# Kernel tuning notes

Hardware: AMD Instinct MI355X
Metric: run time of the kernel (lower is better)

Reference implementation:

```python
import jax, jax.numpy as jnp
import numpy as np

B, C, RXD, E, P, OSIZE = 64, 4, 64, 512, 4, 256


def setup_inputs() -> dict:
    key = jax.random.key(0)
    ks = jax.random.split(key, 6)
    x = jax.random.normal(ks[0], (B, C, RXD, E), dtype=jnp.float32)
    # rxd permutation (gather form of the one-hot permuteRxdMatrix matmul)
    rxd_perm = jax.random.permutation(ks[1], RXD)
    # E permutation and its compositions: permuter = permuter @ permuteEMatrix
    # in column-index form: idx_{p+1}[j] = idx_p[e_perm[j]]
    e_perm = np.array(jax.random.permutation(ks[2], E))
    idx = e_perm.copy()
    cols = []
    for _ in range(P):
        cols.append(idx.copy())
        idx = idx[e_perm]
    e_idx = jnp.asarray(np.stack(cols, axis=1))  # (E, P) int
    # sign selected at the single nonzero entry of each permutation column
    signs = (jax.random.uniform(ks[3], (E, P)) > 0.5).astype(jnp.float32) * 2.0 - 1.0
    fan_in = RXD * E * P
    W = jax.random.normal(ks[4], (OSIZE, fan_in), dtype=jnp.float32) / np.float32(np.sqrt(fan_in))
    b = jax.random.normal(ks[5], (OSIZE,), dtype=jnp.float32) * 0.01
    return {"x": x, "rxd_perm": rxd_perm, "e_idx": e_idx, "signs": signs, "W": W, "b": b}


def reference(x, rxd_perm, e_idx, signs, W, b):
    Bb, Cc, R, Ee = x.shape
    Pp = e_idx.shape[1]
    # permute rxd axis (exact equivalent of x.transpose @ one-hot matrix)
    out = x[:, :, rxd_perm, :]                      # (B,C,R,E)
    # signed E-permutations for all P powers (exact equiv of dense matmul
    # with permuteETensor * signTensor, which has one signed nonzero per column)
    out = out[..., e_idx] * signs                   # (B,C,R,E,P)
    L = R * Ee
    pieces = []
    for p in range(Pp):
        k = 2 ** p
        v = out[..., p].reshape(Bb, Cc, L)
        if k == 1:
            pieces.append(v)                        # pool+unpool with k=1 is identity
        else:
            Lp = ((L + k - 1) // k) * k             # ceil_mode padding
            vp = jnp.pad(v, ((0, 0), (0, 0), (0, Lp - L)), constant_values=-jnp.inf)
            w = vp.reshape(Bb, Cc, Lp // k, k)
            am = jnp.argmax(w, axis=-1)             # first max, matching torch MaxPool1d
            mx = jnp.max(w, axis=-1)
            onehot = jnp.arange(k) == am[..., None]
            # MaxUnpool: max value at argmax position, zeros elsewhere
            pieces.append(jnp.where(onehot, mx[..., None], 0.0).reshape(Bb, Cc, Lp))
    pieces[-1] = pieces[-1][:, :, :L]               # truncate last piece to L
    cat = jnp.concatenate(pieces, axis=2)           # (B,C,L*P) since L % k == 0
    return cat @ W.T + b                            # (B,C,OSIZE)
```

## Files before the change

kernel.cpp:

```cpp
#include <hip/hip_runtime.h>
#include <stdint.h>

#define B_ 64
#define C_ 4
#define R_ 64
#define E_ 512
#define P_ 4
#define OS_ 256
#define L_ (R_*E_)
#define K_ (L_*E8_DUMMY)
#undef K_
#define K_ 131072
#define M_ 256

#define BM 256
#define BN 128
#define BK 32
#define Z_ 256
#define KCH (K_/Z_)
#define ITERS (KCH/BK)

typedef float  floatx4 __attribute__((ext_vector_type(4)));
typedef short  shortx8 __attribute__((ext_vector_type(8)));

#define GLDS16(g, l) __builtin_amdgcn_global_load_lds(                      \
    (const __attribute__((address_space(1))) void*)(g),                     \
    (__attribute__((address_space(3))) void*)(l), 16, 0, 0)

static __device__ __forceinline__ unsigned short f2bf(float f) {
  union { float f; unsigned int u; } v; v.f = f;
  unsigned int u = v.u;
  u += 0x7fffu + ((u >> 16) & 1u);
  return (unsigned short)(u >> 16);
}

__global__ __launch_bounds__(512) void prep(
    const float* __restrict__ x, const int* __restrict__ rxd_perm,
    const int* __restrict__ e_idx, const float* __restrict__ signs,
    const float* __restrict__ W,
    unsigned short* __restrict__ A2, unsigned short* __restrict__ W2) {
  __shared__ __align__(16) unsigned char smem[64 * 33 * 16];
  const int t = threadIdx.x;

  if (blockIdx.x < 2048) {
    const int blk = blockIdx.x;
    const int bcg = blk >> 6;
    const int r   = blk & 63;
    float (*xr)[E_] = (float(*)[E_])smem;
    const int pr = rxd_perm[r];

    #pragma unroll
    for (int i = 0; i < 2; ++i) {
      const int q   = i * 512 + t;
      const int row = q >> 7;
      const int c4  = q & 127;
      const int bc  = bcg * 8 + row;
      *(float4*)(&xr[row][c4 * 4]) =
          *(const float4*)(x + ((size_t)bc * R_ + pr) * E_ + c4 * 4);
    }
    __syncthreads();

    const int bcLoc = t >> 6;
    const int lane  = t & 63;
    const int e0    = lane * 8;
    const int bc    = bcg * 8 + bcLoc;
    const float* xp = xr[bcLoc];

    float v[4][8];
    #pragma unroll
    for (int i = 0; i < 8; ++i) {
      const uint4  ei = *(const uint4*)(e_idx + (size_t)(e0 + i) * 4);
      const float4 sg = *(const float4*)(signs + (size_t)(e0 + i) * 4);
      v[0][i] = xp[ei.x] * sg.x;
      v[1][i] = xp[ei.y] * sg.y;
      v[2][i] = xp[ei.z] * sg.z;
      v[3][i] = xp[ei.w] * sg.w;
    }

    const size_t gbase = (size_t)(r * 64 + lane) * 256 + bc;
    shortx8 o;

    #pragma unroll
    for (int i = 0; i < 8; ++i) o[i] = (short)f2bf(v[0][i]);
    *(shortx8*)(A2 + gbase * 8) = o;

    #pragma unroll
    for (int j = 0; j < 4; ++j) {
      const float a = v[1][2 * j], b = v[1][2 * j + 1];
      const bool first = (a >= b);
      o[2 * j]     = (short)f2bf(first ? a : 0.0f);
      o[2 * j + 1] = (short)f2bf(first ? 0.0f : b);
    }
    *(shortx8*)(A2 + (gbase + (size_t)4096 * 256) * 8) = o;

    #pragma unroll
    for (int j = 0; j < 2; ++j) {
      int am = 0; float m = v[2][4 * j];
      #pragma unroll
      for (int i = 1; i < 4; ++i)
        if (v[2][4 * j + i] > m) { m = v[2][4 * j + i]; am = i; }
      #pragma unroll
      for (int i = 0; i < 4; ++i) o[4 * j + i] = (short)f2bf(i == am ? m : 0.0f);
    }
    *(shortx8*)(A2 + (gbase + (size_t)2 * 4096 * 256) * 8) = o;

    {
      int am = 0; float m = v[3][0];
      #pragma unroll
      for (int i = 1; i < 8; ++i)
        if (v[3][i] > m) { m = v[3][i]; am = i; }
      #pragma unroll
      for (int i = 0; i < 8; ++i) o[i] = (short)f2bf(i == am ? m : 0.0f);
    }
    *(shortx8*)(A2 + (gbase + (size_t)3 * 4096 * 256) * 8) = o;

  } else {
    const int cb = blockIdx.x - 2048;
    const int nb = cb & 7;
    const int kb = cb >> 3;
    const int nbase  = nb * 32;
    const int k8base = kb * 64;
    unsigned short* T = (unsigned short*)smem;

    const int nloc = t >> 4, seg = t & 15;
    const float* wp = W + (size_t)(nbase + nloc) * K_ + (size_t)kb * 512 + seg * 32;
    #pragma unroll
    for (int j = 0; j < 4; ++j) {
      const float4 a0 = *(const float4*)(wp + j * 8);
      const float4 a1 = *(const float4*)(wp + j * 8 + 4);
      shortx8 g;
      g[0] = (short)f2bf(a0.x); g[1] = (short)f2bf(a0.y);
      g[2] = (short)f2bf(a0.z); g[3] = (short)f2bf(a0.w);
      g[4] = (short)f2bf(a1.x); g[5] = (short)f2bf(a1.y);
      g[6] = (short)f2bf(a1.z); g[7] = (short)f2bf(a1.w);
      const int k8loc = seg * 4 + j;
      *(shortx8*)(&T[(k8loc * 33 + nloc) * 8]) = g;
    }
    __syncthreads();

    const int k8loc = t >> 3, part = t & 7;
    unsigned short* wdst = W2 + ((size_t)(k8base + k8loc) * 256 + nbase) * 8;
    #pragma unroll
    for (int j = 0; j < 4; ++j) {
      const int g = j * 8 + part;
      *(shortx8*)(wdst + (size_t)g * 8) = *(const shortx8*)(&T[(k8loc * 33 + g) * 8]);
    }
  }
}

__global__ __launch_bounds__(512, 4) void gemm_splitk(
    const unsigned short* __restrict__ A2, const unsigned short* __restrict__ W2,
    float* __restrict__ Pp) {
  __shared__ unsigned short As[2][4 * 256 * 8];
  __shared__ unsigned short Ws[2][4 * 128 * 8];
  const int t    = threadIdx.x;
  const int lane = t & 63;
  const int wv   = t >> 6;

  const int id = blockIdx.x;
  const int ny = (id >> 3) & 1;
  const int z  = (id & 7) | ((id >> 4) << 3);
  const int nBase = ny * BN;

  const int wm   = (wv >> 1) * 64;
  const int wn   = (wv & 1) * 64;
  const int lrow = lane & 15;
  const int quad = lane >> 4;

  floatx4 acc[4][4];
  #pragma unroll
  for (int i = 0; i < 4; ++i)
    #pragma unroll
    for (int j = 0; j < 4; ++j) acc[i][j] = {0.f, 0.f, 0.f, 0.f};

  auto stage = [&](int buf, int it) {
    const size_t g0 = (size_t)(z * 64 + it * 4) * 256;
    #pragma unroll
    for (int c = 0; c < 2; ++c) {
      const int slot = (wv * 2 + c) * 64 + lane;
      GLDS16(A2 + (g0 + slot) * 8, &As[buf][slot * 8]);
    }
    const int wslot = wv * 64 + lane;
    const int slab  = wslot >> 7;
    const int nloc  = wslot & 127;
    GLDS16(W2 + (g0 + (size_t)slab * 256 + nBase + nloc) * 8, &Ws[buf][wslot * 8]);
  };
  auto compute = [&](int buf) {
    shortx8 af[4], wf[4];
    #pragma unroll
    for (int ti = 0; ti < 4; ++ti)
      af[ti] = *(const shortx8*)(&As[buf][(quad * 256 + wm + ti * 16 + lrow) * 8]);
    #pragma unroll
    for (int tj = 0; tj < 4; ++tj)
      wf[tj] = *(const shortx8*)(&Ws[buf][(quad * 128 + wn + tj * 16 + lrow) * 8]);
    #pragma unroll
    for (int ti = 0; ti < 4; ++ti)
      #pragma unroll
      for (int tj = 0; tj < 4; ++tj)
        acc[ti][tj] = __builtin_amdgcn_mfma_f32_16x16x32_bf16(
            af[ti], wf[tj], acc[ti][tj], 0, 0, 0);
  };

  stage(0, 0);
  __syncthreads();

  for (int it = 0; it < ITERS; ++it) {
    const int b = it & 1;
    if (it + 1 < ITERS) stage(b ^ 1, it + 1);
    compute(b);
    __syncthreads();
  }

  float* Pz = Pp + (size_t)z * (M_ * OS_);
  #pragma unroll
  for (int ti = 0; ti < 4; ++ti)
    #pragma unroll
    for (int tj = 0; tj < 4; ++tj)
      #pragma unroll
      for (int j = 0; j < 4; ++j) {
        const int m = wm + ti * 16 + quad * 4 + j;
        const int n = nBase + wn + tj * 16 + lrow;
        Pz[(size_t)m * OS_ + n] = acc[ti][tj][j];
      }
}

__global__ __launch_bounds__(256) void reduce_out(
    const float* __restrict__ Pp, const float* __restrict__ bias,
    float* __restrict__ out) {
  __shared__ float4 part[128];
  const int t    = threadIdx.x;
  const int i4   = blockIdx.x * 128 + (t & 127);
  const int half = t >> 7;
  const float* p = Pp + (size_t)i4 * 4 + (size_t)half * 128 * (M_ * OS_);
  float4 s = {0.f, 0.f, 0.f, 0.f};
  #pragma unroll 8
  for (int zz = 0; zz < 128; ++zz) {
    const float4 v = *(const float4*)(p + (size_t)zz * (M_ * OS_));
    s.x += v.x; s.y += v.y; s.z += v.z; s.w += v.w;
  }
  if (half) part[t & 127] = s;
  __syncthreads();
  if (!half) {
    const float4 q = part[t];
    const float4 bb = *(const float4*)(bias + ((i4 * 4) & (OS_ - 1)));
    float4 o = {s.x + q.x + bb.x, s.y + q.y + bb.y,
                s.z + q.z + bb.z, s.w + q.w + bb.w};
    *(float4*)(out + (size_t)i4 * 4) = o;
  }
}

extern "C" void kernel_launch(void* const* d_in, const int* in_sizes, int n_in,
                              void* d_out, int out_size, void* d_ws, size_t ws_size,
                              hipStream_t stream) {
  const float* x        = (const float*)d_in[0];
  const int*   rxd_perm = (const int*)d_in[1];
  const int*   e_idx    = (const int*)d_in[2];
  const float* signs    = (const float*)d_in[3];
  const float* W        = (const float*)d_in[4];
  const float* bias     = (const float*)d_in[5];
  float* out = (float*)d_out;

  unsigned short* A2 = (unsigned short*)d_ws;
  unsigned short* W2 = (unsigned short*)((char*)d_ws + 67108864);
  float*          Pp = (float*)((char*)d_ws + 134217728);

  prep<<<dim3(4096), dim3(512), 0, stream>>>(x, rxd_perm, e_idx, signs, W, A2, W2);
  gemm_splitk<<<dim3(2 * Z_), dim3(512), 0, stream>>>(A2, W2, Pp);
  reduce_out<<<dim3(128), dim3(256), 0, stream>>>(Pp, bias, out);
}
```

Measured before the change: 335.0 us.

## Restructure prep kernel: fewer larger blocks, coalesced A2 stores, XOR-swizzled W transpose

The prep kernel is reorganized from 4096 blocks to 768. W-conversion blocks now each handle a full 512-wide K slab across all 256 outputs, using an XOR-swizzled 64KB LDS transpose instead of a padded one. Activation blocks now load 32 bc rows per r and map consecutive threads to consecutive bc, so the bf16 A2 stores become contiguous across lanes. The aim is better store coalescing and less launch and block overhead, at the cost of larger LDS use per block (lower occupancy) and more serial work per block.

```diff
diff --git a/kernel.cpp b/kernel.cpp
--- a/kernel.cpp
+++ b/kernel.cpp
@@ -7,9 +7,7 @@
 #define E_ 512
 #define P_ 4
 #define OS_ 256
-#define L_ (R_*E_)
-#define K_ (L_*E8_DUMMY)
-#undef K_
+#define L_ 32768
 #define K_ 131072
 #define M_ 256
 
@@ -39,111 +37,114 @@
     const int* __restrict__ e_idx, const float* __restrict__ signs,
     const float* __restrict__ W,
     unsigned short* __restrict__ A2, unsigned short* __restrict__ W2) {
-  __shared__ __align__(16) unsigned char smem[64 * 33 * 16];
-  const int t = threadIdx.x;
-
-  if (blockIdx.x < 2048) {
-    const int blk = blockIdx.x;
-    const int bcg = blk >> 6;
-    const int r   = blk & 63;
+  __shared__ __align__(16) unsigned char smem[65536];
+  const int t    = threadIdx.x;
+  const int lane = t & 63;
+  const int wv   = t >> 6;
+
+  if (blockIdx.x < 256) {
+    const int kb = blockIdx.x;
+    unsigned short* T = (unsigned short*)smem;
+
+    #pragma unroll 1
+    for (int nt = 0; nt < 4; ++nt) {
+      const int n0 = nt * 64;
+      #pragma unroll
+      for (int j = 0; j < 8; ++j) {
+        const int n = j * 8 + wv;
+        const float* wp = W + (size_t)(n0 + n) * K_ + (size_t)kb * 512 + lane * 8;
+        const float4 a0 = *(const float4*)(wp);
+        const float4 a1 = *(const float4*)(wp + 4);
+        shortx8 g;
+        g[0] = (short)f2bf(a0.x); g[1] = (short)f2bf(a0.y);
+        g[2] = (short)f2bf(a0.z); g[3] = (short)f2bf(a0.w);
+        g[4] = (short)f2bf(a1.x); g[5] = (short)f2bf(a1.y);
+        g[6] = (short)f2bf(a1.z); g[7] = (short)f2bf(a1.w);
+        *(shortx8*)(&T[((size_t)lane * 64 + (n ^ lane)) * 8]) = g;
+      }
+      __syncthreads();
+      #pragma unroll
+      for (int i = 0; i < 8; ++i) {
+        const int k8loc = wv * 8 + i;
+        const shortx8 g = *(const shortx8*)(&T[((size_t)k8loc * 64 + (lane ^ k8loc)) * 8]);
+        *(shortx8*)(W2 + ((size_t)(kb * 64 + k8loc) * 256 + n0 + lane) * 8) = g;
+      }
+      __syncthreads();
+    }
+
+  } else {
+    const int blk = blockIdx.x - 256;
+    const int r   = blk >> 3;
+    const int bcg = blk & 7;
     float (*xr)[E_] = (float(*)[E_])smem;
     const int pr = rxd_perm[r];
 
     #pragma unroll
-    for (int i = 0; i < 2; ++i) {
+    for (int i = 0; i < 8; ++i) {
       const int q   = i * 512 + t;
       const int row = q >> 7;
       const int c4  = q & 127;
-      const int bc  = bcg * 8 + row;
       *(float4*)(&xr[row][c4 * 4]) =
-          *(const float4*)(x + ((size_t)bc * R_ + pr) * E_ + c4 * 4);
+          *(const float4*)(x + ((size_t)(bcg * 32 + row) * R_ + pr) * E_ + c4 * 4);
     }
     __syncthreads();
 
-    const int bcLoc = t >> 6;
-    const int lane  = t & 63;
-    const int e0    = lane * 8;
-    const int bc    = bcg * 8 + bcLoc;
-    const float* xp = xr[bcLoc];
-
-    float v[4][8];
-    #pragma unroll
-    for (int i = 0; i < 8; ++i) {
-      const uint4  ei = *(const uint4*)(e_idx + (size_t)(e0 + i) * 4);
-      const float4 sg = *(const float4*)(signs + (size_t)(e0 + i) * 4);
-      v[0][i] = xp[ei.x] * sg.x;
-      v[1][i] = xp[ei.y] * sg.y;
-      v[2][i] = xp[ei.z] * sg.z;
-      v[3][i] = xp[ei.w] * sg.w;
-    }
-
-    const size_t gbase = (size_t)(r * 64 + lane) * 256 + bc;
-    shortx8 o;
-
-    #pragma unroll
-    for (int i = 0; i < 8; ++i) o[i] = (short)f2bf(v[0][i]);
-    *(shortx8*)(A2 + gbase * 8) = o;
-
-    #pragma unroll
-    for (int j = 0; j < 4; ++j) {
-      const float a = v[1][2 * j], b = v[1][2 * j + 1];
-      const bool first = (a >= b);
-      o[2 * j]     = (short)f2bf(first ? a : 0.0f);
-      o[2 * j + 1] = (short)f2bf(first ? 0.0f : b);
-    }
-    *(shortx8*)(A2 + (gbase + (size_t)4096 * 256) * 8) = o;
-
-    #pragma unroll
-    for (int j = 0; j < 2; ++j) {
-      int am = 0; float m = v[2][4 * j];
-      #pragma unroll
-      for (int i = 1; i < 4; ++i)
-        if (v[2][4 * j + i] > m) { m = v[2][4 * j + i]; am = i; }
-      #pragma unroll
-      for (int i = 0; i < 4; ++i) o[4 * j + i] = (short)f2bf(i == am ? m : 0.0f);
-    }
-    *(shortx8*)(A2 + (gbase + (size_t)2 * 4096 * 256) * 8) = o;
-
-    {
-      int am = 0; float m = v[3][0];
-      #pragma unroll
-      for (int i = 1; i < 8; ++i)
-        if (v[3][i] > m) { m = v[3][i]; am = i; }
-      #pragma unroll
-      for (int i = 0; i < 8; ++i) o[i] = (short)f2bf(i == am ? m : 0.0f);
-    }
-    *(shortx8*)(A2 + (gbase + (size_t)3 * 4096 * 256) * 8) = o;
-
-  } else {
-    const int cb = blockIdx.x - 2048;
-    const int nb = cb & 7;
-    const int kb = cb >> 3;
-    const int nbase  = nb * 32;
-    const int k8base = kb * 64;
-    unsigned short* T = (unsigned short*)smem;
-
-    const int nloc = t >> 4, seg = t & 15;
-    const float* wp = W + (size_t)(nbase + nloc) * K_ + (size_t)kb * 512 + seg * 32;
-    #pragma unroll
-    for (int j = 0; j < 4; ++j) {
-      const float4 a0 = *(const float4*)(wp + j * 8);
-      const float4 a1 = *(const float4*)(wp + j * 8 + 4);
-      shortx8 g;
-      g[0] = (short)f2bf(a0.x); g[1] = (short)f2bf(a0.y);
-      g[2] = (short)f2bf(a0.z); g[3] = (short)f2bf(a0.w);
-      g[4] = (short)f2bf(a1.x); g[5] = (short)f2bf(a1.y);
-      g[6] = (short)f2bf(a1.z); g[7] = (short)f2bf(a1.w);
-      const int k8loc = seg * 4 + j;
-      *(shortx8*)(&T[(k8loc * 33 + nloc) * 8]) = g;
-    }
-    __syncthreads();
-
-    const int k8loc = t >> 3, part = t & 7;
-    unsigned short* wdst = W2 + ((size_t)(k8base + k8loc) * 256 + nbase) * 8;
-    #pragma unroll
-    for (int j = 0; j < 4; ++j) {
-      const int g = j * 8 + part;
-      *(shortx8*)(wdst + (size_t)g * 8) = *(const shortx8*)(&T[(k8loc * 33 + g) * 8]);
+    const int bcl = t & 31;
+    const int bc  = bcg * 32 + bcl;
+    const float* xp = xr[bcl];
+
+    #pragma unroll 1
+    for (int task = 0; task < 4; ++task) {
+      const int l  = task * 16 + (t >> 5);
+      const int e0 = l * 8;
+
+      float v[4][8];
+      #pragma unroll
+      for (int i = 0; i < 8; ++i) {
+        const uint4  ei = *(const uint4*)(e_idx + (size_t)(e0 + i) * 4);
+        const float4 sg = *(const float4*)(signs + (size_t)(e0 + i) * 4);
+        v[0][i] = xp[ei.x] * sg.x;
+        v[1][i] = xp[ei.y] * sg.y;
+        v[2][i] = xp[ei.z] * sg.z;
+        v[3][i] = xp[ei.w] * sg.w;
+      }
+
+      unsigned short* dst = A2 + ((size_t)(r * 64 + l) * 256 + bc) * 8;
+      shortx8 o;
+
+      #pragma unroll
+      for (int i = 0; i < 8; ++i) o[i] = (short)f2bf(v[0][i]);
+      *(shortx8*)(dst) = o;
+
+      #pragma unroll
+      for (int j = 0; j < 4; ++j) {
+        const float a = v[1][2 * j], b = v[1][2 * j + 1];
+        const bool first = (a >= b);
+        o[2 * j]     = (short)f2bf(first ? a : 0.0f);
+        o[2 * j + 1] = (short)f2bf(first ? 0.0f : b);
+      }
+      *(shortx8*)(dst + (size_t)4096 * 256 * 8) = o;
+
+      #pragma unroll
+      for (int j = 0; j < 2; ++j) {
+        int am = 0; float m = v[2][4 * j];
+        #pragma unroll
+        for (int i = 1; i < 4; ++i)
+          if (v[2][4 * j + i] > m) { m = v[2][4 * j + i]; am = i; }
+        #pragma unroll
+        for (int i = 0; i < 4; ++i) o[4 * j + i] = (short)f2bf(i == am ? m : 0.0f);
+      }
+      *(shortx8*)(dst + (size_t)2 * 4096 * 256 * 8) = o;
+
+      {
+        int am = 0; float m = v[3][0];
+        #pragma unroll
+        for (int i = 1; i < 8; ++i)
+          if (v[3][i] > m) { m = v[3][i]; am = i; }
+        #pragma unroll
+        for (int i = 0; i < 8; ++i) o[i] = (short)f2bf(i == am ? m : 0.0f);
+      }
+      *(shortx8*)(dst + (size_t)3 * 4096 * 256 * 8) = o;
     }
   }
 }
@@ -264,7 +265,7 @@
   unsigned short* W2 = (unsigned short*)((char*)d_ws + 67108864);
   float*          Pp = (float*)((char*)d_ws + 134217728);
 
-  prep<<<dim3(4096), dim3(512), 0, stream>>>(x, rxd_perm, e_idx, signs, W, A2, W2);
+  prep<<<dim3(768), dim3(512), 0, stream>>>(x, rxd_perm, e_idx, signs, W, A2, W2);
   gemm_splitk<<<dim3(2 * Z_), dim3(512), 0, stream>>>(A2, W2, Pp);
   reduce_out<<<dim3(128), dim3(256), 0, stream>>>(Pp, bias, out);
 }
```

Result: no change. 333.2 us (-0.5%).
